# Optimization experiments

Hardware: AMD Instinct MI355X
Metric: run time of the kernel (lower is better)

The kernel has to match this reference:

```python
import jax, jax.numpy as jnp
import numpy as np

NEG_BIG = -9e15
ALPHA = 0.2  # leakyrelu negative slope

N, F_IN, F_OUT = 8192, 512, 64


def setup_inputs() -> dict:
    key = jax.random.key(0)
    k1, k2, k3, k4 = jax.random.split(key, 4)
    input = jax.random.normal(k1, (N, F_IN), dtype=jnp.float32)
    adj = jax.random.randint(k2, (N, N), 0, 2, dtype=jnp.int32)
    W = jax.random.normal(k3, (F_IN, F_OUT), dtype=jnp.float32) * 0.05
    a = jax.random.normal(k4, (2 * F_OUT, 1), dtype=jnp.float32) * 0.1
    return {"input": input, "adj": adj, "W": W, "a": a}


def reference(input, adj, W, a):
    # h: [N, F_out]
    h = input @ W
    # The original builds a_input[i,j] = concat(h_i, h_j) and dots with a.
    # Decompose: e_ij = leakyrelu(h_i @ a_src + h_j @ a_dst) -- identical math,
    # avoids the N*N*2F intermediate.
    a_src = a[:F_OUT, 0]  # [F_out]
    a_dst = a[F_OUT:, 0]  # [F_out]
    s_src = h @ a_src     # [N]
    s_dst = h @ a_dst     # [N]
    e = jax.nn.leaky_relu(s_src[:, None] + s_dst[None, :], negative_slope=ALPHA)  # [N, N]
    masked = jnp.where(adj > 0, e, jnp.float32(NEG_BIG))
    attention = jax.nn.softmax(masked, axis=1)  # dropout omitted (eval mode)
    h_prime = attention @ h  # [N, F_out]
    return jax.nn.elu(h_prime)  # concat=True
```

## Files before the change

kernel.cpp:

```cpp
#include <hip/hip_runtime.h>
#include <hip/hip_bf16.h>

namespace {
constexpr int kN    = 8192;
constexpr int kFin  = 512;
constexpr int kFout = 64;
constexpr float kAlpha = 0.2f;
constexpr int kJSplit = 4;
constexpr int kJLen   = kN / kJSplit;
constexpr int kChunks = kJLen / 128;

using bf16x8 = __attribute__((ext_vector_type(8))) short;
using f32x4  = __attribute__((ext_vector_type(4))) float;

__device__ __forceinline__ unsigned short f2bf(float x) {
  return __builtin_bit_cast(unsigned short, __float2bfloat16(x));
}
__device__ __forceinline__ float lrelu(float x) {
  return fmaxf(x, kAlpha * x);
}
}

__global__ __launch_bounds__(256) void k_wt(const float* __restrict__ W,
                                            float* __restrict__ WT) {
  const int gid = blockIdx.x * 256 + threadIdx.x;
  const int k = gid >> 6, f = gid & 63;
  WT[(size_t)f * kFin + k] = W[gid];
}

__global__ __launch_bounds__(256) void k_linear(
    const float* __restrict__ X, const float* __restrict__ WT, const float* __restrict__ A,
    unsigned short* __restrict__ hTf, float* __restrict__ s_src, float* __restrict__ s_dst)
{
  const int t = threadIdx.x;
  const int rh = t >> 6, f = t & 63;
  const int i0 = blockIdx.x * 8;
  const int r0 = i0 + rh * 2;

  const float* x0 = X + (size_t)r0 * kFin;
  const float* w0 = WT + (size_t)f * kFin;
  float a0 = 0.f, a1 = 0.f;
  for (int k = 0; k < kFin; k += 4) {
    const float4 wv = *(const float4*)(w0 + k);
    const float4 xa = *(const float4*)(x0 + k);
    const float4 xb = *(const float4*)(x0 + kFin + k);
#pragma unroll
    for (int j = 0; j < 4; ++j) {
      a0 = fmaf(((const float*)&xa)[j], ((const float*)&wv)[j], a0);
      a1 = fmaf(((const float*)&xb)[j], ((const float*)&wv)[j], a1);
    }
  }

  const float asrc = A[f], adst = A[kFout + f];
  float accs[2] = {a0, a1};
#pragma unroll
  for (int r = 0; r < 2; ++r) {
    float vs = accs[r] * asrc;
    float vd = accs[r] * adst;
#pragma unroll
    for (int off = 32; off > 0; off >>= 1) {
      vs += __shfl_xor(vs, off, 64);
      vd += __shfl_xor(vd, off, 64);
    }
    if (f == 0) { s_src[r0 + r] = vs; s_dst[r0 + r] = vd; }
  }

  __shared__ unsigned short h_sm[8][64];
  h_sm[rh * 2 + 0][f] = f2bf(a0);
  h_sm[rh * 2 + 1][f] = f2bf(a1);
  __syncthreads();
  if (t < 64) {
    const int w = t >> 4, fl = t & 15;
    const int jblk = i0 >> 5, q = (i0 >> 3) & 3;
    const int lane = q * 16 + fl;
    bf16x8 v;
#pragma unroll
    for (int e = 0; e < 8; ++e) v[e] = (short)h_sm[e][w * 16 + fl];
    *(bf16x8*)(hTf + (((size_t)jblk * 4 + w) * 64 + lane) * 8) = v;
  }
}

__global__ __launch_bounds__(1024) void k_smax(const float* __restrict__ s_dst,
                                               float* __restrict__ Sout)
{
  __shared__ float red[16];
  float m = -3.4e38f;
  for (int i = threadIdx.x; i < kN; i += 1024) m = fmaxf(m, s_dst[i]);
#pragma unroll
  for (int off = 32; off > 0; off >>= 1) m = fmaxf(m, __shfl_xor(m, off, 64));
  if ((threadIdx.x & 63) == 0) red[threadIdx.x >> 6] = m;
  __syncthreads();
  if (threadIdx.x == 0) {
    float s = red[0];
#pragma unroll
    for (int i = 1; i < 16; ++i) s = fmaxf(s, red[i]);
    *Sout = s;
  }
}

__global__ __launch_bounds__(256) void k_attn(
    const int* __restrict__ adj, const unsigned short* __restrict__ hTf,
    const float* __restrict__ s_src, const float* __restrict__ s_dst,
    const float* __restrict__ Sp, float* __restrict__ accp, float* __restrict__ lp)
{
  const int t = threadIdx.x;
  const int wv = t >> 6, lane = t & 63;
  const int b = blockIdx.x;
  const int i0 = (b >> 2) * 16;
  const int jbase = (b & 3) * kJLen;
  const int pr = t >> 4, jb = t & 15;

  __shared__ unsigned short Plds[2][16][136];

  const float S = *Sp;
  const float ssrc = s_src[i0 + pr];
  const float mr = lrelu(ssrc + S);

  float l_acc = 0.f;
  f32x4 acc = {0.f, 0.f, 0.f, 0.f};

  const size_t adj_off = (size_t)(i0 + pr) * kN + jbase + (size_t)jb * 8;
  int4 A0, A1; float4 d0, d1;
  auto load_chunk = [&](int c) {
    const int4* ap = (const int4*)(adj + adj_off + (size_t)c * 128);
    A0 = ap[0]; A1 = ap[1];
    const float* dp = s_dst + jbase + c * 128 + jb * 8;
    d0 = ((const float4*)dp)[0];
    d1 = ((const float4*)dp)[1];
  };
  load_chunk(0);

  const int mrow = lane & 15, quad = lane >> 4;
  const unsigned short* hptr =
      hTf + (((size_t)(jbase >> 5) * 4 + wv) * 64 + lane) * 8;

  for (int c = 0; c < kChunks; ++c) {
    float pv[8];
    {
      const int* aa = (const int*)&A0;
      const float* dd = (const float*)&d0;
#pragma unroll
      for (int j = 0; j < 4; ++j) {
        const float e = lrelu(ssrc + dd[j]);
        pv[j] = aa[j] > 0 ? __expf(e - mr) : 0.f;
      }
      aa = (const int*)&A1; dd = (const float*)&d1;
#pragma unroll
      for (int j = 0; j < 4; ++j) {
        const float e = lrelu(ssrc + dd[j]);
        pv[4 + j] = aa[j] > 0 ? __expf(e - mr) : 0.f;
      }
    }
    bf16x8 ps;
#pragma unroll
    for (int j = 0; j < 8; ++j) {
      l_acc += pv[j];
      ps[j] = (short)f2bf(pv[j]);
    }
    *(bf16x8*)&Plds[c & 1][pr][jb * 8] = ps;
    if (c + 1 < kChunks) load_chunk(c + 1);
    __syncthreads();
#pragma unroll
    for (int ks = 0; ks < 4; ++ks) {
      const bf16x8 av = *(const bf16x8*)&Plds[c & 1][mrow][ks * 32 + quad * 8];
      const bf16x8 bv = *(const bf16x8*)(hptr + ((size_t)c * 4 + ks) * 2048);
      acc = __builtin_amdgcn_mfma_f32_16x16x32_bf16(av, bv, acc, 0, 0, 0);
    }
  }

  float lv = l_acc;
  lv += __shfl_xor(lv, 8, 64);
  lv += __shfl_xor(lv, 4, 64);
  lv += __shfl_xor(lv, 2, 64);
  lv += __shfl_xor(lv, 1, 64);
  if (jb == 0) lp[(size_t)b * 16 + pr] = lv;

  float* ab = accp + (size_t)b * 16 * 64;
#pragma unroll
  for (int reg = 0; reg < 4; ++reg) {
    ab[(quad * 4 + reg) * 64 + wv * 16 + mrow] = acc[reg];
  }
}

__global__ __launch_bounds__(256) void k_comb(const float* __restrict__ accp,
                                              const float* __restrict__ lp,
                                              float* __restrict__ out)
{
  const int gid = blockIdx.x * 256 + threadIdx.x;
  const int i = gid >> 6, f = gid & 63;
  const int ib = i >> 4, il = i & 15;
  const int b0 = ib * kJSplit;
  float a = 0.f, l = 0.f;
#pragma unroll
  for (int q = 0; q < kJSplit; ++q) {
    a += accp[((size_t)(b0 + q) * 16 + il) * 64 + f];
    l += lp[(size_t)(b0 + q) * 16 + il];
  }
  float v = a / l;
  v = v > 0.f ? v : __expf(v) - 1.f;
  out[gid] = v;
}

extern "C" void kernel_launch(void* const* d_in, const int* in_sizes, int n_in,
                              void* d_out, int out_size, void* d_ws, size_t ws_size,
                              hipStream_t stream) {
  const float* X   = (const float*)d_in[0];
  const int*   adj = (const int*)d_in[1];
  const float* W   = (const float*)d_in[2];
  const float* A   = (const float*)d_in[3];
  float* out = (float*)d_out;

  char* ws = (char*)d_ws;
  unsigned short* hTf = (unsigned short*)ws;              ws += (size_t)kN * kFout * 2;
  float* WT    = (float*)ws;                              ws += (size_t)kFout * kFin * 4;
  float* s_src = (float*)ws;                              ws += kN * 4;
  float* s_dst = (float*)ws;                              ws += kN * 4;
  float* Sp    = (float*)ws;                              ws += 256;
  float* accp  = (float*)ws;                              ws += (size_t)(kN / 16) * kJSplit * 16 * 64 * 4;
  float* lp    = (float*)ws;

  k_wt    <<<kFin * kFout / 256, 256, 0, stream>>>(W, WT);
  k_linear<<<kN / 8, 256, 0, stream>>>(X, WT, A, hTf, s_src, s_dst);
  k_smax  <<<1, 1024, 0, stream>>>(s_dst, Sp);
  k_attn  <<<(kN / 16) * kJSplit, 256, 0, stream>>>(adj, hTf, s_src, s_dst, Sp, accp, lp);
  k_comb  <<<kN * kFout / 256, 256, 0, stream>>>(accp, lp, out);
}
```

Before: 458.0 us.

## Fuse max reduction into linear via atomicMax, stage X in LDS, deepen attn prefetch

Removes the single-block k_smax kernel. The s_dst max is now reduced per block in k_linear and combined with an order-preserving uint atomicMax, which is reset in k_wt. k_linear now handles 16 rows per block with X staged in LDS, and each thread computes 4 rows while register-prefetching W. k_attn prefetches adjacency and s_dst two chunks ahead and issues the h loads before the barrier, to hide global latency. This adds 32KB of LDS in k_linear, which may lower occupancy, and adds register pressure from the deeper prefetch.

```diff
diff --git a/kernel.cpp b/kernel.cpp
--- a/kernel.cpp
+++ b/kernel.cpp
@@ -19,42 +19,79 @@
 __device__ __forceinline__ float lrelu(float x) {
   return fmaxf(x, kAlpha * x);
 }
+__device__ __forceinline__ unsigned int fkey(float x) {
+  unsigned int b = __float_as_uint(x);
+  return (b & 0x80000000u) ? ~b : (b | 0x80000000u);
+}
+__device__ __forceinline__ float fdec(unsigned int k) {
+  return (k & 0x80000000u) ? __uint_as_float(k ^ 0x80000000u) : __uint_as_float(~k);
+}
 }
 
 __global__ __launch_bounds__(256) void k_wt(const float* __restrict__ W,
-                                            float* __restrict__ WT) {
+                                            float* __restrict__ WT,
+                                            unsigned int* __restrict__ Smax_u) {
   const int gid = blockIdx.x * 256 + threadIdx.x;
+  if (gid == 0) *Smax_u = 0u;
   const int k = gid >> 6, f = gid & 63;
   WT[(size_t)f * kFin + k] = W[gid];
 }
 
 __global__ __launch_bounds__(256) void k_linear(
     const float* __restrict__ X, const float* __restrict__ WT, const float* __restrict__ A,
-    unsigned short* __restrict__ hTf, float* __restrict__ s_src, float* __restrict__ s_dst)
+    unsigned short* __restrict__ hTf, float* __restrict__ s_src, float* __restrict__ s_dst,
+    unsigned int* __restrict__ Smax_u)
 {
   const int t = threadIdx.x;
-  const int rh = t >> 6, f = t & 63;
-  const int i0 = blockIdx.x * 8;
-  const int r0 = i0 + rh * 2;
-
-  const float* x0 = X + (size_t)r0 * kFin;
+  const int wv = t >> 6, f = t & 63;
+  const int i0 = blockIdx.x * 16;
+
+  __shared__ float Xlds[16 * kFin];
+  __shared__ unsigned short h_sm[16][64];
+  __shared__ float red[4];
+
+  {
+    const float4* Xg = (const float4*)(X + (size_t)i0 * kFin);
+    float4* Xl = (float4*)Xlds;
+    float4 v[8];
+#pragma unroll
+    for (int i = 0; i < 8; ++i) v[i] = Xg[t + i * 256];
+#pragma unroll
+    for (int i = 0; i < 8; ++i) Xl[t + i * 256] = v[i];
+  }
+  __syncthreads();
+
+  const int r0l = wv * 4;
   const float* w0 = WT + (size_t)f * kFin;
-  float a0 = 0.f, a1 = 0.f;
+  float acc0 = 0.f, acc1 = 0.f, acc2 = 0.f, acc3 = 0.f;
+  float4 wb0 = *(const float4*)(w0 + 0);
+  float4 wb1 = *(const float4*)(w0 + 4);
+  const float* xr = Xlds + r0l * kFin;
   for (int k = 0; k < kFin; k += 4) {
-    const float4 wv = *(const float4*)(w0 + k);
-    const float4 xa = *(const float4*)(x0 + k);
-    const float4 xb = *(const float4*)(x0 + kFin + k);
+    const float4 wc = (k & 4) ? wb1 : wb0;
+    if (k + 8 < kFin) {
+      const float4 wn = *(const float4*)(w0 + k + 8);
+      if (k & 4) wb1 = wn; else wb0 = wn;
+    }
+    const float4 xa = *(const float4*)(xr + k);
+    const float4 xb = *(const float4*)(xr + kFin + k);
+    const float4 xc = *(const float4*)(xr + 2 * kFin + k);
+    const float4 xd = *(const float4*)(xr + 3 * kFin + k);
 #pragma unroll
     for (int j = 0; j < 4; ++j) {
-      a0 = fmaf(((const float*)&xa)[j], ((const float*)&wv)[j], a0);
-      a1 = fmaf(((const float*)&xb)[j], ((const float*)&wv)[j], a1);
+      const float wk = ((const float*)&wc)[j];
+      acc0 = fmaf(((const float*)&xa)[j], wk, acc0);
+      acc1 = fmaf(((const float*)&xb)[j], wk, acc1);
+      acc2 = fmaf(((const float*)&xc)[j], wk, acc2);
+      acc3 = fmaf(((const float*)&xd)[j], wk, acc3);
     }
   }
 
   const float asrc = A[f], adst = A[kFout + f];
-  float accs[2] = {a0, a1};
-#pragma unroll
-  for (int r = 0; r < 2; ++r) {
+  float accs[4] = {acc0, acc1, acc2, acc3};
+  float dmax = -3.4e38f;
+#pragma unroll
+  for (int r = 0; r < 4; ++r) {
     float vs = accs[r] * asrc;
     float vd = accs[r] * adst;
 #pragma unroll
@@ -62,46 +99,37 @@
       vs += __shfl_xor(vs, off, 64);
       vd += __shfl_xor(vd, off, 64);
     }
-    if (f == 0) { s_src[r0 + r] = vs; s_dst[r0 + r] = vd; }
-  }
-
-  __shared__ unsigned short h_sm[8][64];
-  h_sm[rh * 2 + 0][f] = f2bf(a0);
-  h_sm[rh * 2 + 1][f] = f2bf(a1);
+    if (f == 0) {
+      s_src[i0 + r0l + r] = vs;
+      s_dst[i0 + r0l + r] = vd;
+      dmax = fmaxf(dmax, vd);
+    }
+    h_sm[r0l + r][f] = f2bf(accs[r]);
+  }
+  if (f == 0) red[wv] = dmax;
   __syncthreads();
-  if (t < 64) {
-    const int w = t >> 4, fl = t & 15;
-    const int jblk = i0 >> 5, q = (i0 >> 3) & 3;
-    const int lane = q * 16 + fl;
+  if (t == 0) {
+    float m = fmaxf(fmaxf(red[0], red[1]), fmaxf(red[2], red[3]));
+    atomicMax(Smax_u, fkey(m));
+  }
+
+  if (t < 128) {
+    const int jblk = i0 >> 5, half = (i0 >> 4) & 1;
+    const int w = t >> 5, li = t & 31;
+    const int lane = half * 32 + li;
+    const int ql = li >> 4, fcol = w * 16 + (li & 15);
     bf16x8 v;
 #pragma unroll
-    for (int e = 0; e < 8; ++e) v[e] = (short)h_sm[e][w * 16 + fl];
-    *(bf16x8*)(hTf + (((size_t)jblk * 4 + w) * 64 + lane) * 8) = v;
-  }
-}
-
-__global__ __launch_bounds__(1024) void k_smax(const float* __restrict__ s_dst,
-                                               float* __restrict__ Sout)
-{
-  __shared__ float red[16];
-  float m = -3.4e38f;
-  for (int i = threadIdx.x; i < kN; i += 1024) m = fmaxf(m, s_dst[i]);
-#pragma unroll
-  for (int off = 32; off > 0; off >>= 1) m = fmaxf(m, __shfl_xor(m, off, 64));
-  if ((threadIdx.x & 63) == 0) red[threadIdx.x >> 6] = m;
-  __syncthreads();
-  if (threadIdx.x == 0) {
-    float s = red[0];
-#pragma unroll
-    for (int i = 1; i < 16; ++i) s = fmaxf(s, red[i]);
-    *Sout = s;
+    for (int e = 0; e < 8; ++e) v[e] = (short)h_sm[ql * 8 + e][fcol];
+    *(bf16x8*)(hTf + (size_t)jblk * 2048 + w * 512 + (size_t)lane * 8) = v;
   }
 }
 
 __global__ __launch_bounds__(256) void k_attn(
     const int* __restrict__ adj, const unsigned short* __restrict__ hTf,
     const float* __restrict__ s_src, const float* __restrict__ s_dst,
-    const float* __restrict__ Sp, float* __restrict__ accp, float* __restrict__ lp)
+    const unsigned int* __restrict__ Smax_u, float* __restrict__ accp,
+    float* __restrict__ lp)
 {
   const int t = threadIdx.x;
   const int wv = t >> 6, lane = t & 63;
@@ -112,39 +140,37 @@
 
   __shared__ unsigned short Plds[2][16][136];
 
-  const float S = *Sp;
+  const float S = fdec(*Smax_u);
   const float ssrc = s_src[i0 + pr];
   const float mr = lrelu(ssrc + S);
 
   float l_acc = 0.f;
   f32x4 acc = {0.f, 0.f, 0.f, 0.f};
 
-  const size_t adj_off = (size_t)(i0 + pr) * kN + jbase + (size_t)jb * 8;
-  int4 A0, A1; float4 d0, d1;
-  auto load_chunk = [&](int c) {
-    const int4* ap = (const int4*)(adj + adj_off + (size_t)c * 128);
-    A0 = ap[0]; A1 = ap[1];
-    const float* dp = s_dst + jbase + c * 128 + jb * 8;
-    d0 = ((const float4*)dp)[0];
-    d1 = ((const float4*)dp)[1];
-  };
-  load_chunk(0);
+  const int4*   aptr = (const int4*)(adj + (size_t)(i0 + pr) * kN + jbase + jb * 8);
+  const float4* dptr = (const float4*)(s_dst + jbase + jb * 8);
+  const unsigned short* hbase = hTf + (size_t)(jbase >> 5) * 2048 + wv * 512 + (size_t)lane * 8;
+
+  int4 A0[2], A1[2]; float4 D0[2], D1[2];
+#pragma unroll
+  for (int s = 0; s < 2; ++s) {
+    A0[s] = aptr[s * 32]; A1[s] = aptr[s * 32 + 1];
+    D0[s] = dptr[s * 32]; D1[s] = dptr[s * 32 + 1];
+  }
 
   const int mrow = lane & 15, quad = lane >> 4;
-  const unsigned short* hptr =
-      hTf + (((size_t)(jbase >> 5) * 4 + wv) * 64 + lane) * 8;
-
   for (int c = 0; c < kChunks; ++c) {
+    const int s = c & 1;
     float pv[8];
     {
-      const int* aa = (const int*)&A0;
-      const float* dd = (const float*)&d0;
+      const int* aa = (const int*)&A0[s];
+      const float* dd = (const float*)&D0[s];
 #pragma unroll
       for (int j = 0; j < 4; ++j) {
         const float e = lrelu(ssrc + dd[j]);
         pv[j] = aa[j] > 0 ? __expf(e - mr) : 0.f;
       }
-      aa = (const int*)&A1; dd = (const float*)&d1;
+      aa = (const int*)&A1[s]; dd = (const float*)&D1[s];
 #pragma unroll
       for (int j = 0; j < 4; ++j) {
         const float e = lrelu(ssrc + dd[j]);
@@ -157,15 +183,27 @@
       l_acc += pv[j];
       ps[j] = (short)f2bf(pv[j]);
     }
-    *(bf16x8*)&Plds[c & 1][pr][jb * 8] = ps;
-    if (c + 1 < kChunks) load_chunk(c + 1);
+    *(bf16x8*)&Plds[s][pr][jb * 8] = ps;
+
+    uint4 hv0 = *(const uint4*)(hbase + (size_t)(c * 4 + 0) * 2048);
+    uint4 hv1 = *(const uint4*)(hbase + (size_t)(c * 4 + 1) * 2048);
+    uint4 hv2 = *(const uint4*)(hbase + (size_t)(c * 4 + 2) * 2048);
+    uint4 hv3 = *(const uint4*)(hbase + (size_t)(c * 4 + 3) * 2048);
+
+    if (c + 2 < kChunks) {
+      A0[s] = aptr[(c + 2) * 32]; A1[s] = aptr[(c + 2) * 32 + 1];
+      D0[s] = dptr[(c + 2) * 32]; D1[s] = dptr[(c + 2) * 32 + 1];
+    }
     __syncthreads();
-#pragma unroll
-    for (int ks = 0; ks < 4; ++ks) {
-      const bf16x8 av = *(const bf16x8*)&Plds[c & 1][mrow][ks * 32 + quad * 8];
-      const bf16x8 bv = *(const bf16x8*)(hptr + ((size_t)c * 4 + ks) * 2048);
-      acc = __builtin_amdgcn_mfma_f32_16x16x32_bf16(av, bv, acc, 0, 0, 0);
-    }
+
+    acc = __builtin_amdgcn_mfma_f32_16x16x32_bf16(
+        *(const bf16x8*)&Plds[s][mrow][0 * 32 + quad * 8], __builtin_bit_cast(bf16x8, hv0), acc, 0, 0, 0);
+    acc = __builtin_amdgcn_mfma_f32_16x16x32_bf16(
+        *(const bf16x8*)&Plds[s][mrow][1 * 32 + quad * 8], __builtin_bit_cast(bf16x8, hv1), acc, 0, 0, 0);
+    acc = __builtin_amdgcn_mfma_f32_16x16x32_bf16(
+        *(const bf16x8*)&Plds[s][mrow][2 * 32 + quad * 8], __builtin_bit_cast(bf16x8, hv2), acc, 0, 0, 0);
+    acc = __builtin_amdgcn_mfma_f32_16x16x32_bf16(
+        *(const bf16x8*)&Plds[s][mrow][3 * 32 + quad * 8], __builtin_bit_cast(bf16x8, hv3), acc, 0, 0, 0);
   }
 
   float lv = l_acc;
@@ -211,17 +249,16 @@
   float* out = (float*)d_out;
 
   char* ws = (char*)d_ws;
-  unsigned short* hTf = (unsigned short*)ws;              ws += (size_t)kN * kFout * 2;
-  float* WT    = (float*)ws;                              ws += (size_t)kFout * kFin * 4;
-  float* s_src = (float*)ws;                              ws += kN * 4;
-  float* s_dst = (float*)ws;                              ws += kN * 4;
-  float* Sp    = (float*)ws;                              ws += 256;
-  float* accp  = (float*)ws;                              ws += (size_t)(kN / 16) * kJSplit * 16 * 64 * 4;
+  unsigned short* hTf = (unsigned short*)ws;  ws += (size_t)kN * kFout * 2;
+  float* WT    = (float*)ws;                  ws += (size_t)kFout * kFin * 4;
+  float* s_src = (float*)ws;                  ws += kN * 4;
+  float* s_dst = (float*)ws;                  ws += kN * 4;
+  unsigned int* Smax_u = (unsigned int*)ws;   ws += 256;
+  float* accp  = (float*)ws;                  ws += (size_t)(kN / 16) * kJSplit * 16 * 64 * 4;
   float* lp    = (float*)ws;
 
-  k_wt    <<<kFin * kFout / 256, 256, 0, stream>>>(W, WT);
-  k_linear<<<kN / 8, 256, 0, stream>>>(X, WT, A, hTf, s_src, s_dst);
-  k_smax  <<<1, 1024, 0, stream>>>(s_dst, Sp);
-  k_attn  <<<(kN / 16) * kJSplit, 256, 0, stream>>>(adj, hTf, s_src, s_dst, Sp, accp, lp);
+  k_wt    <<<kFin * kFout / 256, 256, 0, stream>>>(W, WT, Smax_u);
+  k_linear<<<kN / 16, 256, 0, stream>>>(X, WT, A, hTf, s_src, s_dst, Smax_u);
+  k_attn  <<<(kN / 16) * kJSplit, 256, 0, stream>>>(adj, hTf, s_src, s_dst, Smax_u, accp, lp);
   k_comb  <<<kN * kFout / 256, 256, 0, stream>>>(accp, lp, out);
 }
```

Result: slower. 523.6 us (+14.3%).
